# Kernel tuning notes

Hardware: AMD Instinct MI355X
Metric: run time of the kernel (lower is better)

## Reference

```python
import jax, jax.numpy as jnp
import numpy as np
import math

B, L, S = 2, 2048, 2048
DIN, DK, DV, DOUT, H = 512, 512, 512, 512, 8
HEAD_SIZE = DK / H  # attention_head_size = dim_key_query_all / num_attention_heads


def setup_inputs() -> dict:
    key = jax.random.key(0)
    ks = jax.random.split(key, 12)
    inv = 1.0 / math.sqrt(DIN)
    return {
        "queries": jax.random.normal(ks[0], (B, L, DIN), jnp.float32),
        "keys": jax.random.normal(ks[1], (B, S, DIN), jnp.float32),
        "values": jax.random.normal(ks[2], (B, S, DIN), jnp.float32),
        "attn_mask": 0,
        "Wq": jax.random.uniform(ks[3], (DK, DIN), jnp.float32, -inv, inv),
        "Wk": jax.random.uniform(ks[4], (DK, DIN), jnp.float32, -inv, inv),
        "Wv": jax.random.uniform(ks[5], (DV, DIN), jnp.float32, -inv, inv),
        "bv": jax.random.uniform(ks[6], (DV,), jnp.float32, -inv, inv),
        "Wcb": jax.random.uniform(ks[7], (H, DIN), jnp.float32, -inv, inv),
        "mixing": 0.2 * jax.random.normal(ks[8], (H, DK), jnp.float32),
        "Wd": jax.random.uniform(ks[9], (DOUT, DV), jnp.float32, -1.0 / math.sqrt(DV), 1.0 / math.sqrt(DV)),
        "bd": jax.random.uniform(ks[10], (DOUT,), jnp.float32, -1.0 / math.sqrt(DV), 1.0 / math.sqrt(DV)),
    }


def reference(queries, keys, values, attn_mask, Wq, Wk, Wv, bv, Wcb, mixing, Wd, bd):
    # projections
    q = jnp.einsum('bld,ed->ble', queries, Wq)            # [B,L,DK]
    k = jnp.einsum('bsd,ed->bse', keys, Wk)               # [B,S,DK]
    v = jnp.einsum('bsd,ed->bse', values, Wv) + bv        # [B,S,DV]
    v = v.reshape(B, S, H, DV // H).transpose(0, 2, 1, 3)  # [B,H,S,dv]
    # collaborative scores: (q * mixing_h) @ k^T, per head
    mixed_q = q[:, None, :, :] * mixing[None, :, None, :]  # [B,H,L,DK]
    scores = jnp.einsum('bhle,bse->bhls', mixed_q, k)      # [B,H,L,S]
    # content bias: keys -> [B,S,H] -> broadcast over queries
    cb = jnp.einsum('bsd,hd->bhs', keys, Wcb)              # [B,H,S]
    scores = (scores + cb[:, :, None, :]) / math.sqrt(HEAD_SIZE)
    probs = jax.nn.softmax(scores, axis=-1)                # dropout p=0 (eval)
    ctx = jnp.einsum('bhls,bhsv->bhlv', probs, v)          # [B,H,L,dv]
    ctx = ctx.transpose(0, 2, 1, 3).reshape(B, L, DV)      # [B,L,DV]
    out = jnp.einsum('blv,ov->blo', ctx, Wd) + bd          # [B,L,DOUT]
    return out, probs
```

## Files before the change

### kernel.cpp

```cpp
#include <hip/hip_runtime.h>

typedef unsigned short u16;
typedef __bf16 bf16x8 __attribute__((ext_vector_type(8)));
typedef float floatx4 __attribute__((ext_vector_type(4)));

#define B_ 2
#define L_ 2048
#define S_ 2048
#define D_ 512
#define H_ 8

static __device__ __forceinline__ u16 f2bf(float f) {
  union { float f; unsigned u; } v; v.f = f;
  unsigned u = v.u;
  return (u16)((u + 0x7FFFu + ((u >> 16) & 1u)) >> 16);
}
static __device__ __forceinline__ float bf2f(u16 h) {
  union { unsigned u; float f; } v; v.u = ((unsigned)h) << 16;
  return v.f;
}

__global__ __launch_bounds__(256) void qkv_gemm(
    const float* __restrict__ Qin, const float* __restrict__ Kin, const float* __restrict__ Vin,
    const float* __restrict__ Wq, const float* __restrict__ Wk, const float* __restrict__ Wv,
    const float* __restrict__ bv,
    u16* __restrict__ qo, u16* __restrict__ ko, u16* __restrict__ vo)
{
  __shared__ u16 As[128][72];
  __shared__ u16 Bs[128][72];
  const int z = blockIdx.z;
  const float* A = (z == 0) ? Qin : (z == 1) ? Kin : Vin;
  const float* W = (z == 0) ? Wq : (z == 1) ? Wk : Wv;
  const int tid = threadIdx.x;
  const int m0 = blockIdx.y * 128;
  const int n0 = blockIdx.x * 128;
  const int lane = tid & 63, w = tid >> 6;
  const int ml = lane & 15, kl = lane >> 4;
  const int mqw = (w >> 1) * 64, nq = (w & 1) * 64;
  const int srow = tid >> 4, scg = tid & 15;

  floatx4 acc[4][4] = {};

  for (int k0 = 0; k0 < 512; k0 += 64) {
#pragma unroll
    for (int i = 0; i < 8; ++i) {
      const int r = srow + i * 16;
      float4 av = *(const float4*)&A[(size_t)(m0 + r) * 512 + k0 + scg * 4];
      ushort4 ua; ua.x = f2bf(av.x); ua.y = f2bf(av.y); ua.z = f2bf(av.z); ua.w = f2bf(av.w);
      *(ushort4*)&As[r][scg * 4] = ua;
      float4 wv = *(const float4*)&W[(size_t)(n0 + r) * 512 + k0 + scg * 4];
      ushort4 uw; uw.x = f2bf(wv.x); uw.y = f2bf(wv.y); uw.z = f2bf(wv.z); uw.w = f2bf(wv.w);
      *(ushort4*)&Bs[r][scg * 4] = uw;
    }
    __syncthreads();
#pragma unroll
    for (int kk = 0; kk < 64; kk += 32) {
      bf16x8 af[4], bfv[4];
#pragma unroll
      for (int i = 0; i < 4; ++i) af[i] = *(const bf16x8*)&As[mqw + i * 16 + ml][kk + kl * 8];
#pragma unroll
      for (int j = 0; j < 4; ++j) bfv[j] = *(const bf16x8*)&Bs[nq + j * 16 + ml][kk + kl * 8];
#pragma unroll
      for (int i = 0; i < 4; ++i)
#pragma unroll
        for (int j = 0; j < 4; ++j)
          acc[i][j] = __builtin_amdgcn_mfma_f32_16x16x32_bf16(af[i], bfv[j], acc[i][j], 0, 0, 0);
    }
    __syncthreads();
  }
#pragma unroll
  for (int i = 0; i < 4; ++i)
#pragma unroll
    for (int j = 0; j < 4; ++j) {
      const int gc = n0 + nq + j * 16 + ml;
#pragma unroll
      for (int r = 0; r < 4; ++r) {
        const int gr = m0 + mqw + i * 16 + kl * 4 + r;
        float v = acc[i][j][r];
        if (z == 0)      qo[(size_t)gr * 512 + gc] = f2bf(v);
        else if (z == 1) ko[(size_t)gr * 512 + gc] = f2bf(v);
        else             vo[(size_t)gr * 512 + gc] = f2bf(v + bv[gc]);
      }
    }
}

__global__ __launch_bounds__(256) void mixq_kernel(
    const u16* __restrict__ qb, const float* __restrict__ mixing, u16* __restrict__ mq)
{
  __shared__ float mixs[8 * 512];
  const int tid = threadIdx.x;
#pragma unroll
  for (int i = 0; i < 4; ++i)
    *(float4*)&mixs[(tid + i * 256) * 4] = *(const float4*)&mixing[(tid + i * 256) * 4];
  __syncthreads();
  const size_t unit = (size_t)blockIdx.x * 256 + tid;
  const size_t el = unit * 8;
  const int e = (int)(el & 511);
  const size_t bl = el >> 9;
  const int b = (int)(bl >> 11);
  const int l = (int)(bl & 2047);
  uint4 qv = *(const uint4*)&qb[el];
  const float q0 = bf2f((u16)(qv.x & 0xFFFFu)), q1 = bf2f((u16)(qv.x >> 16));
  const float q2 = bf2f((u16)(qv.y & 0xFFFFu)), q3 = bf2f((u16)(qv.y >> 16));
  const float q4 = bf2f((u16)(qv.z & 0xFFFFu)), q5 = bf2f((u16)(qv.z >> 16));
  const float q6 = bf2f((u16)(qv.w & 0xFFFFu)), q7 = bf2f((u16)(qv.w >> 16));
#pragma unroll
  for (int h = 0; h < 8; ++h) {
    const float* mp = &mixs[h * 512 + e];
    uint4 o;
    o.x = (unsigned)f2bf(q0 * mp[0]) | ((unsigned)f2bf(q1 * mp[1]) << 16);
    o.y = (unsigned)f2bf(q2 * mp[2]) | ((unsigned)f2bf(q3 * mp[3]) << 16);
    o.z = (unsigned)f2bf(q4 * mp[4]) | ((unsigned)f2bf(q5 * mp[5]) << 16);
    o.w = (unsigned)f2bf(q6 * mp[6]) | ((unsigned)f2bf(q7 * mp[7]) << 16);
    *(uint4*)&mq[(((size_t)b * 8 + h) * 2048 + l) * 512 + e] = o;
  }
}

__global__ __launch_bounds__(256) void out_gemm(
    const float* __restrict__ A, const float* __restrict__ W,
    const float* __restrict__ bias, float* __restrict__ out)
{
  __shared__ u16 As[128][72];
  __shared__ u16 Bs[128][72];
  const int tid = threadIdx.x;
  const int m0 = blockIdx.y * 128;
  const int n0 = blockIdx.x * 128;
  const int lane = tid & 63, w = tid >> 6;
  const int ml = lane & 15, kl = lane >> 4;
  const int mqw = (w >> 1) * 64, nq = (w & 1) * 64;
  const int srow = tid >> 4, scg = tid & 15;

  floatx4 acc[4][4] = {};

  for (int k0 = 0; k0 < 512; k0 += 64) {
#pragma unroll
    for (int i = 0; i < 8; ++i) {
      const int r = srow + i * 16;
      float4 av = *(const float4*)&A[(size_t)(m0 + r) * 512 + k0 + scg * 4];
      ushort4 ua; ua.x = f2bf(av.x); ua.y = f2bf(av.y); ua.z = f2bf(av.z); ua.w = f2bf(av.w);
      *(ushort4*)&As[r][scg * 4] = ua;
      float4 wv = *(const float4*)&W[(size_t)(n0 + r) * 512 + k0 + scg * 4];
      ushort4 uw; uw.x = f2bf(wv.x); uw.y = f2bf(wv.y); uw.z = f2bf(wv.z); uw.w = f2bf(wv.w);
      *(ushort4*)&Bs[r][scg * 4] = uw;
    }
    __syncthreads();
#pragma unroll
    for (int kk = 0; kk < 64; kk += 32) {
      bf16x8 af[4], bfv[4];
#pragma unroll
      for (int i = 0; i < 4; ++i) af[i] = *(const bf16x8*)&As[mqw + i * 16 + ml][kk + kl * 8];
#pragma unroll
      for (int j = 0; j < 4; ++j) bfv[j] = *(const bf16x8*)&Bs[nq + j * 16 + ml][kk + kl * 8];
#pragma unroll
      for (int i = 0; i < 4; ++i)
#pragma unroll
        for (int j = 0; j < 4; ++j)
          acc[i][j] = __builtin_amdgcn_mfma_f32_16x16x32_bf16(af[i], bfv[j], acc[i][j], 0, 0, 0);
    }
    __syncthreads();
  }
#pragma unroll
  for (int i = 0; i < 4; ++i)
#pragma unroll
    for (int j = 0; j < 4; ++j) {
      const int gc = n0 + nq + j * 16 + ml;
#pragma unroll
      for (int r = 0; r < 4; ++r) {
        const int gr = m0 + mqw + i * 16 + kl * 4 + r;
        out[(size_t)gr * 512 + gc] = acc[i][j][r] + bias[gc];
      }
    }
}

__global__ __launch_bounds__(256) void cb_kernel(
    const float* __restrict__ keys, const float* __restrict__ Wcb, float* __restrict__ cbuf)
{
  __shared__ float Wl[8 * 512];
  const int tid = threadIdx.x;
#pragma unroll
  for (int i = 0; i < 4; ++i) {
    const int idx = tid + i * 256;
    *(float4*)&Wl[idx * 4] = *(const float4*)&Wcb[idx * 4];
  }
  __syncthreads();
  const int w = tid >> 6, lane = tid & 63;
  const int rowid = blockIdx.x * 4 + w;
  const int b = rowid >> 11, s = rowid & 2047;
  const float* kr = keys + (size_t)rowid * 512;
  float acc[8] = {0.f, 0.f, 0.f, 0.f, 0.f, 0.f, 0.f, 0.f};
  for (int e = lane; e < 512; e += 64) {
    const float kv = kr[e];
#pragma unroll
    for (int hh = 0; hh < 8; ++hh) acc[hh] += kv * Wl[hh * 512 + e];
  }
#pragma unroll
  for (int hh = 0; hh < 8; ++hh) {
#pragma unroll
    for (int off = 32; off > 0; off >>= 1) acc[hh] += __shfl_xor(acc[hh], off, 64);
  }
  if (lane == 0) {
#pragma unroll
    for (int hh = 0; hh < 8; ++hh)
      cbuf[((size_t)b * 8 + hh) * 2048 + s] = acc[hh];
  }
}

__global__ __launch_bounds__(256) void transpose_v(
    const u16* __restrict__ vb, u16* __restrict__ vT)
{
  __shared__ u16 t[64][72];
  const int tid = threadIdx.x;
  const int e0 = blockIdx.x * 64;
  const int s0 = blockIdx.y * 64;
  const int b = blockIdx.z;
  const int rr = tid >> 3, g = tid & 7;
#pragma unroll
  for (int i = 0; i < 2; ++i) {
    const int r = rr + i * 32;
    *(uint4*)&t[r][g * 8] = *(const uint4*)&vb[((size_t)b * S_ + s0 + r) * 512 + e0 + g * 8];
  }
  __syncthreads();
#pragma unroll
  for (int i = 0; i < 2; ++i) {
    const int er = rr + i * 32;
    uint4 o;
    o.x = (unsigned)t[g * 8 + 0][er] | ((unsigned)t[g * 8 + 1][er] << 16);
    o.y = (unsigned)t[g * 8 + 2][er] | ((unsigned)t[g * 8 + 3][er] << 16);
    o.z = (unsigned)t[g * 8 + 4][er] | ((unsigned)t[g * 8 + 5][er] << 16);
    o.w = (unsigned)t[g * 8 + 6][er] | ((unsigned)t[g * 8 + 7][er] << 16);
    *(uint4*)&vT[((size_t)b * 512 + e0 + er) * S_ + s0 + g * 8] = o;
  }
}

__global__ __launch_bounds__(256) void scores_gemm(
    const u16* __restrict__ mq, const u16* __restrict__ kb,
    const float* __restrict__ cbuf, float* __restrict__ sc)
{
  __shared__ u16 As[128][72];
  __shared__ u16 Bs[128][72];
  const int tid = threadIdx.x;
  const int bh = blockIdx.z, b = bh >> 3;
  const int m0 = blockIdx.y * 128;
  const int n0 = blockIdx.x * 128;
  const u16* mqb = mq + (size_t)bh * L_ * 512;
  const u16* kbb = kb + (size_t)b * S_ * 512;
  const int lane = tid & 63, w = tid >> 6;
  const int ml = lane & 15, kl = lane >> 4;
  const int mqw = (w >> 1) * 64, nq = (w & 1) * 64;
  const int brow = tid >> 3, bcg = tid & 7;

  floatx4 acc[4][4] = {};

  for (int k0 = 0; k0 < 512; k0 += 64) {
#pragma unroll
    for (int i = 0; i < 4; ++i) {
      const int r = brow + i * 32;
      *(uint4*)&As[r][bcg * 8] = *(const uint4*)&mqb[(size_t)(m0 + r) * 512 + k0 + bcg * 8];
      *(uint4*)&Bs[r][bcg * 8] = *(const uint4*)&kbb[(size_t)(n0 + r) * 512 + k0 + bcg * 8];
    }
    __syncthreads();
#pragma unroll
    for (int kk = 0; kk < 64; kk += 32) {
      bf16x8 af[4], bfv[4];
#pragma unroll
      for (int i = 0; i < 4; ++i) af[i] = *(const bf16x8*)&As[mqw + i * 16 + ml][kk + kl * 8];
#pragma unroll
      for (int j = 0; j < 4; ++j) bfv[j] = *(const bf16x8*)&Bs[nq + j * 16 + ml][kk + kl * 8];
#pragma unroll
      for (int i = 0; i < 4; ++i)
#pragma unroll
        for (int j = 0; j < 4; ++j)
          acc[i][j] = __builtin_amdgcn_mfma_f32_16x16x32_bf16(af[i], bfv[j], acc[i][j], 0, 0, 0);
    }
    __syncthreads();
  }
  float* outp = sc + ((size_t)bh * L_ + m0) * S_ + n0;
#pragma unroll
  for (int j = 0; j < 4; ++j) {
    const int gcl = nq + j * 16 + ml;
    const float cbv = cbuf[(size_t)bh * S_ + n0 + gcl];
#pragma unroll
    for (int i = 0; i < 4; ++i)
#pragma unroll
      for (int r = 0; r < 4; ++r) {
        const int grl = mqw + i * 16 + kl * 4 + r;
        outp[(size_t)grl * S_ + gcl] = (acc[i][j][r] + cbv) * 0.125f;
      }
  }
}

__global__ __launch_bounds__(256) void softmax_ctx(
    float* __restrict__ sc, const u16* __restrict__ vT, float* __restrict__ ctx)
{
  __shared__ u16 Ps[16][1032];
  const int tid = threadIdx.x;
  const int bh = blockIdx.y, b = bh >> 3, h = bh & 7;
  const int l0 = blockIdx.x * 16;
  float* Sg = sc + ((size_t)bh * L_ + l0) * S_;
  const int row = tid >> 4, jg = tid & 15;

  unsigned pr[64];
  float mx = -3.0e38f;
#pragma unroll
  for (int i = 0; i < 32; ++i) {
    const int c = jg * 4 + i * 64;
    float4 v = *(const float4*)&Sg[(size_t)row * S_ + c];
    pr[2 * i]     = (unsigned)f2bf(v.x) | ((unsigned)f2bf(v.y) << 16);
    pr[2 * i + 1] = (unsigned)f2bf(v.z) | ((unsigned)f2bf(v.w) << 16);
    mx = fmaxf(mx, fmaxf(fmaxf(v.x, v.y), fmaxf(v.z, v.w)));
  }
#pragma unroll
  for (int off = 8; off > 0; off >>= 1) mx = fmaxf(mx, __shfl_xor(mx, off, 64));
  float ls = 0.f;
#pragma unroll
  for (int i = 0; i < 64; ++i) {
    const unsigned u = pr[i];
    ls += __expf(bf2f((u16)(u & 0xFFFFu)) - mx) + __expf(bf2f((u16)(u >> 16)) - mx);
  }
#pragma unroll
  for (int off = 8; off > 0; off >>= 1) ls += __shfl_xor(ls, off, 64);
  const float rl = 1.0f / ls;

  const int lane = tid & 63, wv = tid >> 6;
  const int ml = lane & 15, kl = lane >> 4;
  const u16* vrow = vT + ((size_t)b * 512 + h * 64 + wv * 16 + ml) * S_ + kl * 8;
  floatx4 acc = {};

#pragma unroll
  for (int half = 0; half < 2; ++half) {
    __syncthreads();
#pragma unroll
    for (int i = 0; i < 16; ++i) {
      const int ig = i + half * 16;
      const unsigned u0 = pr[2 * ig], u1 = pr[2 * ig + 1];
      float4 p;
      p.x = __expf(bf2f((u16)(u0 & 0xFFFFu)) - mx) * rl;
      p.y = __expf(bf2f((u16)(u0 >> 16)) - mx) * rl;
      p.z = __expf(bf2f((u16)(u1 & 0xFFFFu)) - mx) * rl;
      p.w = __expf(bf2f((u16)(u1 >> 16)) - mx) * rl;
      const int lc = jg * 4 + i * 64;
      *(float4*)&Sg[(size_t)row * S_ + half * 1024 + lc] = p;
      uint2 t;
      t.x = (unsigned)f2bf(p.x) | ((unsigned)f2bf(p.y) << 16);
      t.y = (unsigned)f2bf(p.z) | ((unsigned)f2bf(p.w) << 16);
      *(uint2*)&Ps[row][lc] = t;
    }
    __syncthreads();
    const u16* vk = vrow + half * 1024;
#pragma unroll
    for (int k0 = 0; k0 < 1024; k0 += 32) {
      bf16x8 a  = *(const bf16x8*)&Ps[ml][k0 + kl * 8];
      bf16x8 bb = *(const bf16x8*)&vk[k0];
      acc = __builtin_amdgcn_mfma_f32_16x16x32_bf16(a, bb, acc, 0, 0, 0);
    }
  }
#pragma unroll
  for (int r = 0; r < 4; ++r)
    ctx[((size_t)b * L_ + l0 + kl * 4 + r) * 512 + h * 64 + wv * 16 + ml] = acc[r];
}

extern "C" void kernel_launch(void* const* d_in, const int* in_sizes, int n_in,
                              void* d_out, int out_size, void* d_ws, size_t ws_size,
                              hipStream_t stream) {
  const float* queries = (const float*)d_in[0];
  const float* keys    = (const float*)d_in[1];
  const float* values  = (const float*)d_in[2];
  const float* Wq  = (const float*)d_in[4];
  const float* Wk  = (const float*)d_in[5];
  const float* Wv  = (const float*)d_in[6];
  const float* bv  = (const float*)d_in[7];
  const float* Wcb = (const float*)d_in[8];
  const float* mixing = (const float*)d_in[9];
  const float* Wd  = (const float*)d_in[10];
  const float* bd  = (const float*)d_in[11];

  float* out   = (float*)d_out;
  float* probs = out + (size_t)B_ * L_ * 512;

  char* ws = (char*)d_ws;
  u16*   qb  = (u16*)(ws);
  u16*   kb  = (u16*)(ws + (size_t)4  * 1024 * 1024);
  u16*   vb  = (u16*)(ws + (size_t)8  * 1024 * 1024);
  u16*   vT  = (u16*)(ws + (size_t)12 * 1024 * 1024);
  float* cbuf= (float*)(ws + (size_t)16 * 1024 * 1024);
  float* ctx = (float*)(ws + (size_t)17 * 1024 * 1024);
  u16*   mq  = (u16*)(ws + (size_t)25 * 1024 * 1024);

  hipLaunchKernelGGL(qkv_gemm, dim3(4, 32, 3), dim3(256), 0, stream,
                     queries, keys, values, Wq, Wk, Wv, bv, qb, kb, vb);
  hipLaunchKernelGGL(mixq_kernel, dim3(1024), dim3(256), 0, stream, qb, mixing, mq);
  hipLaunchKernelGGL(cb_kernel, dim3(1024), dim3(256), 0, stream, keys, Wcb, cbuf);
  hipLaunchKernelGGL(transpose_v, dim3(8, 32, 2), dim3(256), 0, stream, vb, vT);
  hipLaunchKernelGGL(scores_gemm, dim3(16, 16, 16), dim3(256), 0, stream,
                     mq, kb, cbuf, probs);
  hipLaunchKernelGGL(softmax_ctx, dim3(128, 16), dim3(256), 0, stream,
                     probs, vT, ctx);
  hipLaunchKernelGGL(out_gemm, dim3(4, 32, 1), dim3(256), 0, stream,
                     ctx, Wd, bd, out);
}
```

Before: 676.3 us.

## Split softmax and ctx GEMM, store bf16 scores, split-K ctx with atomics

Scores are written as bf16 to a separate workspace buffer when the workspace is large enough, halving the scores write and read traffic. A streaming softmax kernel, one wavefront per row, then writes fp32 probs. A separate split-K ctx GEMM re-reads probs, converts them to bf16 and accumulates into a zeroed ctx buffer with atomics. This replaces the fused softmax_ctx kernel, whose low occupancy and serial MFMA chain were the bottleneck, at the cost of an extra full read of probs, atomic contention, and an extra zeroing launch.

```diff
diff --git a/kernel.cpp b/kernel.cpp
--- a/kernel.cpp
+++ b/kernel.cpp
@@ -232,9 +232,10 @@
   }
 }
 
+template<int BF16OUT>
 __global__ __launch_bounds__(256) void scores_gemm(
     const u16* __restrict__ mq, const u16* __restrict__ kb,
-    const float* __restrict__ cbuf, float* __restrict__ sc)
+    const float* __restrict__ cbuf, float* __restrict__ sc, u16* __restrict__ sb)
 {
   __shared__ u16 As[128][72];
   __shared__ u16 Bs[128][72];
@@ -274,89 +275,150 @@
     }
     __syncthreads();
   }
-  float* outp = sc + ((size_t)bh * L_ + m0) * S_ + n0;
+  if constexpr (BF16OUT) {
+    u16* outp = sb + ((size_t)bh * L_ + m0) * S_ + n0;
+#pragma unroll
+    for (int j = 0; j < 4; ++j) {
+      const int gcl = nq + j * 16 + ml;
+      const float cbv = cbuf[(size_t)bh * S_ + n0 + gcl];
+#pragma unroll
+      for (int i = 0; i < 4; ++i)
+#pragma unroll
+        for (int r = 0; r < 4; ++r) {
+          const int grl = mqw + i * 16 + kl * 4 + r;
+          outp[(size_t)grl * S_ + gcl] = f2bf((acc[i][j][r] + cbv) * 0.125f);
+        }
+    }
+  } else {
+    float* outp = sc + ((size_t)bh * L_ + m0) * S_ + n0;
+#pragma unroll
+    for (int j = 0; j < 4; ++j) {
+      const int gcl = nq + j * 16 + ml;
+      const float cbv = cbuf[(size_t)bh * S_ + n0 + gcl];
+#pragma unroll
+      for (int i = 0; i < 4; ++i)
+#pragma unroll
+        for (int r = 0; r < 4; ++r) {
+          const int grl = mqw + i * 16 + kl * 4 + r;
+          outp[(size_t)grl * S_ + gcl] = (acc[i][j][r] + cbv) * 0.125f;
+        }
+    }
+  }
+}
+
+template<int BF16IN>
+__global__ __launch_bounds__(256) void softmax_stream(
+    const u16* __restrict__ sb, float* probs)
+{
+  const int tid = threadIdx.x;
+  const int row = blockIdx.x * 4 + (tid >> 6);
+  const int lane = tid & 63;
+  float s[32];
+  if constexpr (BF16IN) {
+    const u16* rp = sb + (size_t)row * 2048;
+#pragma unroll
+    for (int j = 0; j < 8; ++j) {
+      uint2 v = *(const uint2*)&rp[lane * 4 + j * 256];
+      s[4 * j + 0] = bf2f((u16)(v.x & 0xFFFFu));
+      s[4 * j + 1] = bf2f((u16)(v.x >> 16));
+      s[4 * j + 2] = bf2f((u16)(v.y & 0xFFFFu));
+      s[4 * j + 3] = bf2f((u16)(v.y >> 16));
+    }
+  } else {
+    const float* rp = probs + (size_t)row * 2048;
+#pragma unroll
+    for (int j = 0; j < 8; ++j) {
+      float4 v = *(const float4*)&rp[lane * 4 + j * 256];
+      s[4 * j + 0] = v.x; s[4 * j + 1] = v.y; s[4 * j + 2] = v.z; s[4 * j + 3] = v.w;
+    }
+  }
+  float m = -3.0e38f;
+#pragma unroll
+  for (int i = 0; i < 32; ++i) m = fmaxf(m, s[i]);
+#pragma unroll
+  for (int off = 32; off > 0; off >>= 1) m = fmaxf(m, __shfl_xor(m, off, 64));
+  float s0 = 0.f, s1 = 0.f, s2 = 0.f, s3 = 0.f;
+#pragma unroll
+  for (int i = 0; i < 32; i += 4) {
+    s[i + 0] = __expf(s[i + 0] - m); s0 += s[i + 0];
+    s[i + 1] = __expf(s[i + 1] - m); s1 += s[i + 1];
+    s[i + 2] = __expf(s[i + 2] - m); s2 += s[i + 2];
+    s[i + 3] = __expf(s[i + 3] - m); s3 += s[i + 3];
+  }
+  float sum = (s0 + s1) + (s2 + s3);
+#pragma unroll
+  for (int off = 32; off > 0; off >>= 1) sum += __shfl_xor(sum, off, 64);
+  const float rl = 1.0f / sum;
+  float* op = probs + (size_t)row * 2048;
+#pragma unroll
+  for (int j = 0; j < 8; ++j) {
+    float4 o;
+    o.x = s[4 * j + 0] * rl; o.y = s[4 * j + 1] * rl;
+    o.z = s[4 * j + 2] * rl; o.w = s[4 * j + 3] * rl;
+    *(float4*)&op[lane * 4 + j * 256] = o;
+  }
+}
+
+__global__ __launch_bounds__(256) void ctx_gemm(
+    const float* __restrict__ probs, const u16* __restrict__ vT, float* __restrict__ ctx)
+{
+  __shared__ u16 As[64][72];
+  __shared__ u16 Bs[64][72];
+  const int tid = threadIdx.x;
+  const int bh = blockIdx.z, b = bh >> 3, h = bh & 7;
+  const int m0 = blockIdx.x * 64;
+  const int kz = blockIdx.y;
+  const float* Ap = probs + ((size_t)bh * L_ + m0) * S_;
+  const u16* Bp = vT + ((size_t)b * 512 + h * 64) * S_;
+  const int lane = tid & 63, w = tid >> 6;
+  const int ml = lane & 15, kl = lane >> 4;
+  const int srow = tid >> 4, scg = tid & 15;
+  const int brow = tid >> 3, bcg = tid & 7;
+
+  floatx4 acc[4] = {};
+
+  const int kend = kz * 1024 + 1024;
+  for (int k0 = kz * 1024; k0 < kend; k0 += 64) {
+#pragma unroll
+    for (int i = 0; i < 4; ++i) {
+      const int r = srow + i * 16;
+      float4 av = *(const float4*)&Ap[(size_t)r * S_ + k0 + scg * 4];
+      ushort4 ua; ua.x = f2bf(av.x); ua.y = f2bf(av.y); ua.z = f2bf(av.z); ua.w = f2bf(av.w);
+      *(ushort4*)&As[r][scg * 4] = ua;
+    }
+#pragma unroll
+    for (int i = 0; i < 2; ++i) {
+      const int r = brow + i * 32;
+      *(uint4*)&Bs[r][bcg * 8] = *(const uint4*)&Bp[(size_t)r * S_ + k0 + bcg * 8];
+    }
+    __syncthreads();
+#pragma unroll
+    for (int kk = 0; kk < 64; kk += 32) {
+      bf16x8 af = *(const bf16x8*)&As[w * 16 + ml][kk + kl * 8];
+#pragma unroll
+      for (int j = 0; j < 4; ++j) {
+        bf16x8 bfv = *(const bf16x8*)&Bs[j * 16 + ml][kk + kl * 8];
+        acc[j] = __builtin_amdgcn_mfma_f32_16x16x32_bf16(af, bfv, acc[j], 0, 0, 0);
+      }
+    }
+    __syncthreads();
+  }
 #pragma unroll
   for (int j = 0; j < 4; ++j) {
-    const int gcl = nq + j * 16 + ml;
-    const float cbv = cbuf[(size_t)bh * S_ + n0 + gcl];
-#pragma unroll
-    for (int i = 0; i < 4; ++i)
-#pragma unroll
-      for (int r = 0; r < 4; ++r) {
-        const int grl = mqw + i * 16 + kl * 4 + r;
-        outp[(size_t)grl * S_ + gcl] = (acc[i][j][r] + cbv) * 0.125f;
-      }
-  }
-}
-
-__global__ __launch_bounds__(256) void softmax_ctx(
-    float* __restrict__ sc, const u16* __restrict__ vT, float* __restrict__ ctx)
-{
-  __shared__ u16 Ps[16][1032];
-  const int tid = threadIdx.x;
-  const int bh = blockIdx.y, b = bh >> 3, h = bh & 7;
-  const int l0 = blockIdx.x * 16;
-  float* Sg = sc + ((size_t)bh * L_ + l0) * S_;
-  const int row = tid >> 4, jg = tid & 15;
-
-  unsigned pr[64];
-  float mx = -3.0e38f;
-#pragma unroll
-  for (int i = 0; i < 32; ++i) {
-    const int c = jg * 4 + i * 64;
-    float4 v = *(const float4*)&Sg[(size_t)row * S_ + c];
-    pr[2 * i]     = (unsigned)f2bf(v.x) | ((unsigned)f2bf(v.y) << 16);
-    pr[2 * i + 1] = (unsigned)f2bf(v.z) | ((unsigned)f2bf(v.w) << 16);
-    mx = fmaxf(mx, fmaxf(fmaxf(v.x, v.y), fmaxf(v.z, v.w)));
-  }
-#pragma unroll
-  for (int off = 8; off > 0; off >>= 1) mx = fmaxf(mx, __shfl_xor(mx, off, 64));
-  float ls = 0.f;
-#pragma unroll
-  for (int i = 0; i < 64; ++i) {
-    const unsigned u = pr[i];
-    ls += __expf(bf2f((u16)(u & 0xFFFFu)) - mx) + __expf(bf2f((u16)(u >> 16)) - mx);
-  }
-#pragma unroll
-  for (int off = 8; off > 0; off >>= 1) ls += __shfl_xor(ls, off, 64);
-  const float rl = 1.0f / ls;
-
-  const int lane = tid & 63, wv = tid >> 6;
-  const int ml = lane & 15, kl = lane >> 4;
-  const u16* vrow = vT + ((size_t)b * 512 + h * 64 + wv * 16 + ml) * S_ + kl * 8;
-  floatx4 acc = {};
-
-#pragma unroll
-  for (int half = 0; half < 2; ++half) {
-    __syncthreads();
-#pragma unroll
-    for (int i = 0; i < 16; ++i) {
-      const int ig = i + half * 16;
-      const unsigned u0 = pr[2 * ig], u1 = pr[2 * ig + 1];
-      float4 p;
-      p.x = __expf(bf2f((u16)(u0 & 0xFFFFu)) - mx) * rl;
-      p.y = __expf(bf2f((u16)(u0 >> 16)) - mx) * rl;
-      p.z = __expf(bf2f((u16)(u1 & 0xFFFFu)) - mx) * rl;
-      p.w = __expf(bf2f((u16)(u1 >> 16)) - mx) * rl;
-      const int lc = jg * 4 + i * 64;
-      *(float4*)&Sg[(size_t)row * S_ + half * 1024 + lc] = p;
-      uint2 t;
-      t.x = (unsigned)f2bf(p.x) | ((unsigned)f2bf(p.y) << 16);
-      t.y = (unsigned)f2bf(p.z) | ((unsigned)f2bf(p.w) << 16);
-      *(uint2*)&Ps[row][lc] = t;
-    }
-    __syncthreads();
-    const u16* vk = vrow + half * 1024;
-#pragma unroll
-    for (int k0 = 0; k0 < 1024; k0 += 32) {
-      bf16x8 a  = *(const bf16x8*)&Ps[ml][k0 + kl * 8];
-      bf16x8 bb = *(const bf16x8*)&vk[k0];
-      acc = __builtin_amdgcn_mfma_f32_16x16x32_bf16(a, bb, acc, 0, 0, 0);
-    }
-  }
-#pragma unroll
-  for (int r = 0; r < 4; ++r)
-    ctx[((size_t)b * L_ + l0 + kl * 4 + r) * 512 + h * 64 + wv * 16 + ml] = acc[r];
+    const int gc = h * 64 + j * 16 + ml;
+#pragma unroll
+    for (int r = 0; r < 4; ++r) {
+      const int gl = m0 + w * 16 + kl * 4 + r;
+      atomicAdd(&ctx[((size_t)b * L_ + gl) * 512 + gc], acc[j][r]);
+    }
+  }
+}
+
+__global__ __launch_bounds__(256) void zero_ctx(float* __restrict__ p)
+{
+  const size_t i = ((size_t)blockIdx.x * 256 + threadIdx.x) * 4;
+  float4 z; z.x = 0.f; z.y = 0.f; z.z = 0.f; z.w = 0.f;
+  *(float4*)&p[i] = z;
 }
 
 extern "C" void kernel_launch(void* const* d_in, const int* in_sizes, int n_in,
@@ -385,16 +447,29 @@
   float* cbuf= (float*)(ws + (size_t)16 * 1024 * 1024);
   float* ctx = (float*)(ws + (size_t)17 * 1024 * 1024);
   u16*   mq  = (u16*)(ws + (size_t)25 * 1024 * 1024);
+  const size_t SB16_OFF = (size_t)57 * 1024 * 1024;
+  const size_t SB16_SZ  = (size_t)B_ * H_ * L_ * S_ * 2;
+  u16* sb16 = (u16*)(ws + SB16_OFF);
+  const bool bigws = (ws_size >= SB16_OFF + SB16_SZ);
 
   hipLaunchKernelGGL(qkv_gemm, dim3(4, 32, 3), dim3(256), 0, stream,
                      queries, keys, values, Wq, Wk, Wv, bv, qb, kb, vb);
   hipLaunchKernelGGL(mixq_kernel, dim3(1024), dim3(256), 0, stream, qb, mixing, mq);
   hipLaunchKernelGGL(cb_kernel, dim3(1024), dim3(256), 0, stream, keys, Wcb, cbuf);
   hipLaunchKernelGGL(transpose_v, dim3(8, 32, 2), dim3(256), 0, stream, vb, vT);
-  hipLaunchKernelGGL(scores_gemm, dim3(16, 16, 16), dim3(256), 0, stream,
-                     mq, kb, cbuf, probs);
-  hipLaunchKernelGGL(softmax_ctx, dim3(128, 16), dim3(256), 0, stream,
-                     probs, vT, ctx);
+  hipLaunchKernelGGL(zero_ctx, dim3(2048), dim3(256), 0, stream, ctx);
+  if (bigws) {
+    hipLaunchKernelGGL(HIP_KERNEL_NAME(scores_gemm<1>), dim3(16, 16, 16), dim3(256), 0, stream,
+                       mq, kb, cbuf, probs, sb16);
+    hipLaunchKernelGGL(HIP_KERNEL_NAME(softmax_stream<1>), dim3(8192), dim3(256), 0, stream,
+                       sb16, probs);
+  } else {
+    hipLaunchKernelGGL(HIP_KERNEL_NAME(scores_gemm<0>), dim3(16, 16, 16), dim3(256), 0, stream,
+                       mq, kb, cbuf, probs, sb16);
+    hipLaunchKernelGGL(HIP_KERNEL_NAME(softmax_stream<0>), dim3(8192), dim3(256), 0, stream,
+                       sb16, probs);
+  }
+  hipLaunchKernelGGL(ctx_gemm, dim3(32, 2, 16), dim3(256), 0, stream, probs, vT, ctx);
   hipLaunchKernelGGL(out_gemm, dim3(4, 32, 1), dim3(256), 0, stream,
                      ctx, Wd, bd, out);
 }
```

Result: faster. 586.6 us (-13.3%).
